# Performance work log

Measured on AMD Instinct MI355X. Metric: run time of the kernel, lower is better.

## Reference

```python
import jax, jax.numpy as jnp
import numpy as np
from jax import lax

NC = 32
EPS = 1e-12


def unfold3x3(x):
    # x: [B,C,H,W] -> [B, C*9, H*W], matching F.unfold(kernel=3, padding=1)
    B, C, H, W = x.shape
    xp = jnp.pad(x, ((0, 0), (0, 0), (1, 1), (1, 1)))
    patches = jnp.stack([xp[:, :, i:i + H, j:j + W]
                         for i in range(3) for j in range(3)], axis=2)  # [B,C,9,H,W]
    return patches.reshape(B, C * 9, H * W)


def fold3x3(u, H, W):
    # u: [B, C*9, H*W] -> [B, C, H, W], matching F.fold(kernel=3, padding=1)
    B = u.shape[0]
    C = u.shape[1] // 9
    p = u.reshape(B, C, 3, 3, H, W)
    out = jnp.zeros((B, C, H + 2, W + 2), u.dtype)
    for i in range(3):
        for j in range(3):
            out = out.at[:, :, i:i + H, j:j + W].add(p[:, :, i, j])
    return out[:, :, 1:H + 1, 1:W + 1]


def l2norm(x, axis):
    n = jnp.sqrt(jnp.sum(x * x, axis=axis, keepdims=True))
    return x / jnp.maximum(n, EPS)


def conv3x3(x, w, b):
    y = lax.conv_general_dilated(x, w, (1, 1), 'SAME',
                                 dimension_numbers=('NCHW', 'OIHW', 'NCHW'))
    return y + b[None, :, None, None]


def setup_inputs() -> dict:
    key = jax.random.key(0)
    k = jax.random.split(key, 6)
    B, C, H, W = 2, NC, 80, 80
    in_HSI = jax.random.normal(k[0], (B, C, H, W), jnp.float32)
    in_PAN = jax.random.normal(k[1], (B, C, H, W), jnp.float32)
    fan1 = 2 * C * 9
    fan2 = C * 9
    w1 = jax.random.normal(k[2], (C, 2 * C, 3, 3), jnp.float32) / np.sqrt(fan1)
    b1 = jax.random.normal(k[3], (C,), jnp.float32) * 0.01
    w2 = jax.random.normal(k[4], (C, C, 3, 3), jnp.float32) / np.sqrt(fan2)
    b2 = jax.random.normal(k[5], (C,), jnp.float32) * 0.01
    return {"in_HSI": in_HSI, "in_PAN": in_PAN, "w1": w1, "b1": b1, "w2": w2, "b2": b2}


def reference(in_HSI, in_PAN, w1, b1, w2, b2):
    B, C, H, W = in_HSI.shape
    L = H * W
    HSI_unfold = unfold3x3(in_HSI)                      # [B, C*9, L]
    PAN_unfold = unfold3x3(in_PAN)                      # [B, C*9, L]
    PAN_q = l2norm(jnp.transpose(PAN_unfold, (0, 2, 1)), axis=2)  # [B, L, C*9]
    HSI_k = l2norm(HSI_unfold, axis=1)                  # [B, C*9, L]
    R = jnp.einsum('blc,bcm->blm', PAN_q, HSI_k)        # [B, L, L]
    R_star = jnp.max(R, axis=1)                         # [B, L]
    R_arg = jnp.argmax(R, axis=1)                       # [B, L]
    # gather columns of unfold(in_PAN) selected by 1-NN indices
    T_unfold = jnp.take_along_axis(PAN_unfold, R_arg[:, None, :], axis=2)
    T_lv3 = fold3x3(T_unfold, H, W) / 9.0               # [B, C, H, W]
    S = R_star.reshape(B, 1, H, W)
    h = jax.nn.relu(conv3x3(jnp.concatenate([T_lv3, in_HSI], axis=1), w1, b1))
    res = conv3x3(h, w2, b2) * S + in_HSI
    return res
```

## Files before the change

### kernel.cpp

```cpp
#include <hip/hip_runtime.h>
#include <hip/hip_bf16.h>
#include <hip/hip_fp16.h>
#include <stdint.h>

#define HH 80
#define WW 80
#define LL 6400
#define CC 32
#define BB 2
#define COG 16
#define DELTA 0.011f
#define NT8 800

typedef __bf16 bf16x8 __attribute__((ext_vector_type(8)));
typedef float  f32x4  __attribute__((ext_vector_type(4)));

__device__ __forceinline__ int div80(int v) {
    return (int)(((unsigned)v * 52429u) >> 22);
}

__device__ __forceinline__ unsigned short f2bf(float f) {
    unsigned int u = __float_as_uint(f);
    return (unsigned short)((u + 0x7fffu + ((u >> 16) & 1u)) >> 16);
}

__device__ __forceinline__ void gload_lds16(void* g, void* l) {
    __builtin_amdgcn_global_load_lds(
        (__attribute__((address_space(1))) void*)g,
        (__attribute__((address_space(3))) void*)l, 16, 0, 0);
}

__global__ void prep1_kernel(const float* __restrict__ HSI, const float* __restrict__ PAN,
                             float* __restrict__ partH, float* __restrict__ partP) {
    int g = blockIdx.x * 256 + threadIdx.x;
    if (g >= BB * CC * LL) return;
    int l = g % LL;
    int y = div80(l), x = l - y * 80;
    const float* hc = HSI + (size_t)(g - l);
    const float* pc = PAN + (size_t)(g - l);
    float sh = 0.f, sp = 0.f;
    #pragma unroll
    for (int i = 0; i < 3; ++i) {
        int yy = y + i - 1;
        if ((unsigned)yy >= 80u) continue;
        #pragma unroll
        for (int j = 0; j < 3; ++j) {
            int xx = x + j - 1;
            if ((unsigned)xx >= 80u) continue;
            float hv = hc[yy * 80 + xx]; sh = fmaf(hv, hv, sh);
            float pv = pc[yy * 80 + xx]; sp = fmaf(pv, pv, sp);
        }
    }
    partH[g] = sh;
    partP[g] = sp;
}

__global__ void prep2_kernel(const float* __restrict__ partH, const float* __restrict__ partP,
                             float* __restrict__ invH, float* __restrict__ invP) {
    int g = blockIdx.x * 256 + threadIdx.x;
    if (g >= BB * LL) return;
    int b = g / LL, l = g - b * LL;
    float sh = 0.f, sp = 0.f;
    #pragma unroll
    for (int c = 0; c < CC; ++c) {
        sh += partH[((size_t)(b * CC + c)) * LL + l];
        sp += partP[((size_t)(b * CC + c)) * LL + l];
    }
    invH[g] = 1.f / fmaxf(sqrtf(sh), 1e-12f);
    invP[g] = 1.f / fmaxf(sqrtf(sp), 1e-12f);
}

__global__ void pack_kernel(const float* __restrict__ HSI, const float* __restrict__ PAN,
                            const float* __restrict__ invH, const float* __restrict__ invP,
                            char* __restrict__ Apack, char* __restrict__ Bpack,
                            float* __restrict__ PANunf, float* __restrict__ HSIunf) {
    int t = blockIdx.x * 256 + threadIdx.x;
    if (t >= BB * 2 * LL * 36) return;
    int g = t % 36;
    int rest = t / 36;
    int l = rest % LL; rest /= LL;
    int mat = rest & 1;
    int b = rest >> 1;
    const float* img = (mat ? HSI : PAN) + (size_t)b * CC * LL;
    float inv = (mat ? invH : invP)[b * LL + l];
    int y = div80(l), x = l - y * 80;
    int k0 = g * 8;
    int c = k0 / 9, tap = k0 - c * 9;
    unsigned short hs[8];
    float raw[8];
    #pragma unroll
    for (int j = 0; j < 8; ++j) {
        int t3 = tap / 3;
        int dy = t3 - 1, dx = tap - t3 * 3 - 1;
        int yy = y + dy, xx = x + dx;
        float rv = ((unsigned)yy < 80u && (unsigned)xx < 80u)
                       ? img[(size_t)c * LL + yy * 80 + xx] : 0.f;
        raw[j] = rv;
        hs[j] = f2bf(rv * inv);
        if (++tap == 9) { tap = 0; ++c; }
    }
    float* unf = (mat ? HSIunf : PANunf) + ((size_t)b * LL + l) * 288 + k0;
    float4 r0 = {raw[0], raw[1], raw[2], raw[3]};
    float4 r1 = {raw[4], raw[5], raw[6], raw[7]};
    *(float4*)(unf)     = r0;
    *(float4*)(unf + 4) = r1;
    char* pk = mat ? Bpack : Apack;
    int slot = (g % 12) ^ (l & 15);
    int q = g / 12;
    size_t off = ((size_t)(b * 3 + q) * LL + l) * 256 + slot * 16;
    uint4 hv;
    hv.x = hs[0] | ((unsigned)hs[1] << 16); hv.y = hs[2] | ((unsigned)hs[3] << 16);
    hv.z = hs[4] | ((unsigned)hs[5] << 16); hv.w = hs[6] | ((unsigned)hs[7] << 16);
    *(uint4*)(pk + off) = hv;
}

__global__ __launch_bounds__(256, 2) void simq_kernel(const char* __restrict__ Apack,
                                                      const char* __restrict__ Bpack,
                                                      __half* __restrict__ tileMax8) {
    __shared__ __align__(16) char Alds[2][32768];
    const int orig = blockIdx.x;
    const int xcd = orig & 7, idx = orig >> 3;
    const int wg = (xcd < 4 ? xcd * 63 : 252 + (xcd - 4) * 62) + idx;
    const int b = wg / 250;
    int rest = wg - b * 250;
    const int sp = rest / 50;
    const int mt = rest - sp * 50;

    const int tid = threadIdx.x;
    const int lane = tid & 63, w = tid >> 6;
    const int wl = w >> 1, wm = w & 1;
    const int r15 = lane & 15, h = lane >> 4;
    const char* Ab = Apack + (size_t)b * 3 * LL * 256;
    const char* Bb = Bpack + (size_t)b * 3 * LL * 256;
    const int m0 = mt * 128;
    const f32x4 fzero = {0.f, 0.f, 0.f, 0.f};

    bf16x8 bq[3][3][4];
    {
        const int rowb = m0 + wm * 64 + r15;
        #pragma unroll
        for (int c = 0; c < 3; ++c)
            #pragma unroll
            for (int ks = 0; ks < 3; ++ks)
                #pragma unroll
                for (int fm = 0; fm < 4; ++fm) {
                    const int gp = ((ks * 4 + h) ^ r15) * 16;
                    bq[c][ks][fm] = *(const bf16x8*)(Bb + ((size_t)c * LL + rowb + fm * 16) * 256 + gp);
                }
    }

    {
        const char* gA = Ab + ((size_t)(sp * 10) * 128) * 256 + w * 8192 + lane * 16;
        char* lA = Alds[0] + w * 8192;
        #pragma unroll
        for (int i = 0; i < 8; ++i) gload_lds16((void*)(gA + i * 1024), lA + i * 1024);
    }
    __syncthreads();

    int cur = 0;
    #pragma unroll 1
    for (int lt = 0; lt < 10; ++lt) {
        f32x4 acc[4][4];
        #pragma unroll
        for (int i = 0; i < 4; ++i)
            #pragma unroll
            for (int j = 0; j < 4; ++j) acc[i][j] = fzero;

        #pragma unroll
        for (int c = 0; c < 3; ++c) {
            if (c < 2 || lt < 9) {
                const int lt2 = (c == 2) ? lt + 1 : lt;
                const int c2  = (c == 2) ? 0 : c + 1;
                const int l0n = (sp * 10 + lt2) * 128;
                const char* gA = Ab + ((size_t)c2 * LL + l0n) * 256 + w * 8192 + lane * 16;
                char* lA = Alds[cur ^ 1] + w * 8192;
                #pragma unroll
                for (int i = 0; i < 8; ++i) gload_lds16((void*)(gA + i * 1024), lA + i * 1024);
            }
            const char* lAr = Alds[cur];
            #pragma unroll
            for (int ks = 0; ks < 3; ++ks) {
                const int gp = ((ks * 4 + h) ^ r15) * 16;
                bf16x8 af[4];
                #pragma unroll
                for (int f = 0; f < 4; ++f)
                    af[f] = *(const bf16x8*)(lAr + (wl * 64 + f * 16 + r15) * 256 + gp);
                #pragma unroll
                for (int fl = 0; fl < 4; ++fl)
                    #pragma unroll
                    for (int fm = 0; fm < 4; ++fm)
                        acc[fl][fm] = __builtin_amdgcn_mfma_f32_16x16x32_bf16(
                            af[fl], bq[c][ks][fm], acc[fl][fm], 0, 0, 0);
            }
            __syncthreads();
            cur ^= 1;
        }

        const int Tbase = (sp * 10 + lt) * 16 + wl * 8;
        #pragma unroll
        for (int fl = 0; fl < 4; ++fl) {
            #pragma unroll
            for (int fm = 0; fm < 4; ++fm) {
                f32x4 a = acc[fl][fm];
                float v = fmaxf(fmaxf(a[0], a[1]), fmaxf(a[2], a[3]));
                v = fmaxf(v, __shfl_xor(v, 16, 64));
                if ((h & 1) == 0) {
                    const int m = m0 + wm * 64 + fm * 16 + r15;
                    tileMax8[((size_t)b * LL + m) * NT8 + Tbase + fl * 2 + (h >> 1)] = __float2half(v);
                }
            }
        }
    }
}

__global__ __launch_bounds__(256) void scanfix_kernel(const float* __restrict__ PANunf,
                                                      const float* __restrict__ HSIunf,
                                                      const float* __restrict__ invH,
                                                      const float* __restrict__ invP,
                                                      const __half* __restrict__ tileMax8,
                                                      float* __restrict__ Sv, int* __restrict__ Sa) {
    const int gw = blockIdx.x * 4 + (threadIdx.x >> 6);
    const int lane = threadIdx.x & 63;
    const int b = gw / LL;
    const __half* tm = tileMax8 + (size_t)gw * NT8;

    float tv[13];
    #pragma unroll
    for (int i = 0; i < 13; ++i) {
        int T = i * 64 + lane;
        tv[i] = (T < NT8) ? __half2float(tm[T]) : -3.0e38f;
    }
    float v1 = tv[0];
    #pragma unroll
    for (int i = 1; i < 13; ++i) v1 = fmaxf(v1, tv[i]);
    #pragma unroll
    for (int d = 1; d < 64; d <<= 1) v1 = fmaxf(v1, __shfl_xor(v1, d, 64));
    const float th = v1 - DELTA;

    const float ihm = invH[gw];
    const int lql = lane >> 3, kq = lane & 7;

    float hreg[36];
    {
        const float4* hv4 = (const float4*)(HSIunf + (size_t)gw * 288 + kq * 36);
        #pragma unroll
        for (int j = 0; j < 9; ++j) {
            float4 v = hv4[j];
            hreg[j * 4 + 0] = v.x; hreg[j * 4 + 1] = v.y;
            hreg[j * 4 + 2] = v.z; hreg[j * 4 + 3] = v.w;
        }
    }

    float bv = -3.0e38f; int bl = 0x7fffffff;

    #pragma unroll 1
    for (int i = 0; i < 13; ++i) {
        unsigned long long mask = __ballot(tv[i] >= th);
        while (mask) {
            const int t = __ffsll((long long)mask) - 1;
            mask &= mask - 1;
            const int T = i * 64 + t;
            const int l = T * 8 + lql;
            const float4* pv4 = (const float4*)(PANunf + ((size_t)b * LL + l) * 288 + kq * 36);
            float part = 0.f;
            #pragma unroll
            for (int j = 0; j < 9; ++j) {
                float4 p = pv4[j];
                part = fmaf(p.x, hreg[j * 4 + 0], part);
                part = fmaf(p.y, hreg[j * 4 + 1], part);
                part = fmaf(p.z, hreg[j * 4 + 2], part);
                part = fmaf(p.w, hreg[j * 4 + 3], part);
            }
            part += __shfl_xor(part, 1, 64);
            part += __shfl_xor(part, 2, 64);
            part += __shfl_xor(part, 4, 64);
            const float val = part * invP[b * LL + l] * ihm;
            if (val > bv || (val == bv && l < bl)) { bv = val; bl = l; }
        }
    }
    #pragma unroll
    for (int d = 1; d < 64; d <<= 1) {
        float ov = __shfl_xor(bv, d, 64);
        int   ol = __shfl_xor(bl, d, 64);
        if (ov > bv || (ov == bv && ol < bl)) { bv = ov; bl = ol; }
    }
    if (lane == 0) { Sv[gw] = bv; Sa[gw] = bl; }
}

__global__ void tfold_kernel(const float* __restrict__ PAN, const int* __restrict__ Sa,
                             float* __restrict__ T) {
    int g = blockIdx.x * blockDim.x + threadIdx.x;
    if (g >= BB * CC * LL) return;
    int bc = g / LL, l = g - bc * LL;
    int b = bc >> 5;
    int y = div80(l), x = l - y * 80;
    const float* img = PAN + (size_t)bc * LL;
    const int* Sab = Sa + b * LL;
    float acc = 0.f;
    #pragma unroll
    for (int i = 0; i < 3; ++i) {
        int yp = y + 1 - i;
        if ((unsigned)yp >= 80u) continue;
        #pragma unroll
        for (int j = 0; j < 3; ++j) {
            int xp = x + 1 - j;
            if ((unsigned)xp >= 80u) continue;
            int a = Sab[yp * 80 + xp];
            int ya = div80(a), xa = a - ya * 80;
            int py = ya + i - 1, px = xa + j - 1;
            if ((unsigned)py < 80u && (unsigned)px < 80u) acc += img[py * 80 + px];
        }
    }
    T[g] = acc * (1.f / 9.f);
}

__global__ __launch_bounds__(256) void conv1_kernel(const float* __restrict__ T,
                                                    const float* __restrict__ HSI,
                                                    const float* __restrict__ w1,
                                                    const float* __restrict__ b1,
                                                    float* __restrict__ h) {
    __shared__ __align__(16) float wl[64][9][COG];
    const int tid = threadIdx.x;
    const int co0 = blockIdx.y * COG;
    for (int idx = tid; idx < 64 * 9 * COG; idx += 256) {
        int cog = idx & (COG - 1);
        int rest = idx >> 4;
        int cin = rest / 9, tap = rest - cin * 9;
        wl[cin][tap][cog] = w1[(co0 + cog) * (64 * 9) + cin * 9 + tap];
    }
    __syncthreads();
    const int g = blockIdx.x * 256 + tid;
    const int b = g / LL, l = g - b * LL;
    const int y = div80(l), x = l - y * 80;
    float acc[COG];
    #pragma unroll
    for (int i = 0; i < COG; ++i) acc[i] = 0.f;
    for (int cin = 0; cin < 64; ++cin) {
        const float* img = (cin < CC) ? (T + (size_t)(b * CC + cin) * LL)
                                      : (HSI + (size_t)(b * CC + (cin - CC)) * LL);
        float tap[9];
        #pragma unroll
        for (int i = 0; i < 3; ++i)
            #pragma unroll
            for (int j = 0; j < 3; ++j) {
                int yy = y + i - 1, xx = x + j - 1;
                tap[i * 3 + j] = ((unsigned)yy < 80u && (unsigned)xx < 80u) ? img[yy * 80 + xx] : 0.f;
            }
        #pragma unroll
        for (int t9 = 0; t9 < 9; ++t9) {
            #pragma unroll
            for (int q4 = 0; q4 < COG / 4; ++q4) {
                const float4 wv = *reinterpret_cast<const float4*>(&wl[cin][t9][q4 * 4]);
                acc[q4 * 4 + 0] = fmaf(tap[t9], wv.x, acc[q4 * 4 + 0]);
                acc[q4 * 4 + 1] = fmaf(tap[t9], wv.y, acc[q4 * 4 + 1]);
                acc[q4 * 4 + 2] = fmaf(tap[t9], wv.z, acc[q4 * 4 + 2]);
                acc[q4 * 4 + 3] = fmaf(tap[t9], wv.w, acc[q4 * 4 + 3]);
            }
        }
    }
    #pragma unroll
    for (int cog = 0; cog < COG; ++cog) {
        float v = acc[cog] + b1[co0 + cog];
        h[(size_t)(b * CC + co0 + cog) * LL + l] = fmaxf(v, 0.f);
    }
}

__global__ __launch_bounds__(256) void conv2_kernel(const float* __restrict__ hbuf,
                                                    const float* __restrict__ HSI,
                                                    const float* __restrict__ Sv,
                                                    const float* __restrict__ w2,
                                                    const float* __restrict__ b2,
                                                    float* __restrict__ out) {
    __shared__ __align__(16) float wl[CC][9][COG];
    const int tid = threadIdx.x;
    const int co0 = blockIdx.y * COG;
    for (int idx = tid; idx < CC * 9 * COG; idx += 256) {
        int cog = idx & (COG - 1);
        int rest = idx >> 4;
        int cin = rest / 9, tap = rest - cin * 9;
        wl[cin][tap][cog] = w2[(co0 + cog) * (CC * 9) + cin * 9 + tap];
    }
    __syncthreads();
    const int g = blockIdx.x * 256 + tid;
    const int b = g / LL, l = g - b * LL;
    const int y = div80(l), x = l - y * 80;
    float acc[COG];
    #pragma unroll
    for (int i = 0; i < COG; ++i) acc[i] = 0.f;
    for (int cin = 0; cin < CC; ++cin) {
        const float* img = hbuf + (size_t)(b * CC + cin) * LL;
        float tap[9];
        #pragma unroll
        for (int i = 0; i < 3; ++i)
            #pragma unroll
            for (int j = 0; j < 3; ++j) {
                int yy = y + i - 1, xx = x + j - 1;
                tap[i * 3 + j] = ((unsigned)yy < 80u && (unsigned)xx < 80u) ? img[yy * 80 + xx] : 0.f;
            }
        #pragma unroll
        for (int t9 = 0; t9 < 9; ++t9) {
            #pragma unroll
            for (int q4 = 0; q4 < COG / 4; ++q4) {
                const float4 wv = *reinterpret_cast<const float4*>(&wl[cin][t9][q4 * 4]);
                acc[q4 * 4 + 0] = fmaf(tap[t9], wv.x, acc[q4 * 4 + 0]);
                acc[q4 * 4 + 1] = fmaf(tap[t9], wv.y, acc[q4 * 4 + 1]);
                acc[q4 * 4 + 2] = fmaf(tap[t9], wv.z, acc[q4 * 4 + 2]);
                acc[q4 * 4 + 3] = fmaf(tap[t9], wv.w, acc[q4 * 4 + 3]);
            }
        }
    }
    const float s = Sv[b * LL + l];
    #pragma unroll
    for (int cog = 0; cog < COG; ++cog) {
        int c = co0 + cog;
        out[(size_t)(b * CC + c) * LL + l] = fmaf(acc[cog] + b2[c], s, HSI[(size_t)(b * CC + c) * LL + l]);
    }
}

extern "C" void kernel_launch(void* const* d_in, const int* in_sizes, int n_in,
                              void* d_out, int out_size, void* d_ws, size_t ws_size,
                              hipStream_t stream) {
    const float* HSI = (const float*)d_in[0];
    const float* PAN = (const float*)d_in[1];
    const float* w1  = (const float*)d_in[2];
    const float* b1  = (const float*)d_in[3];
    const float* w2  = (const float*)d_in[4];
    const float* b2  = (const float*)d_in[5];
    float* out = (float*)d_out;

    char* ws = (char*)d_ws;
    size_t off = 0;
    auto alloc = [&](size_t bytes) -> void* {
        void* p = ws + off;
        off += (bytes + 255) & ~(size_t)255;
        return p;
    };
    float* partH = (float*)alloc((size_t)BB * CC * LL * 4);
    float* partP = (float*)alloc((size_t)BB * CC * LL * 4);
    float* invH  = (float*)alloc((size_t)BB * LL * 4);
    float* invP  = (float*)alloc((size_t)BB * LL * 4);
    char*  Apack = (char*) alloc((size_t)BB * 3 * LL * 256);
    char*  Bpack = (char*) alloc((size_t)BB * 3 * LL * 256);
    __half* tileMax8 = (__half*)alloc((size_t)BB * LL * NT8 * 2);
    float* PANunf = (float*)alloc((size_t)BB * LL * 288 * 4);
    float* HSIunf = (float*)alloc((size_t)BB * LL * 288 * 4);
    float* Sv    = (float*)alloc((size_t)BB * LL * 4);
    int*   Sa    = (int*)  alloc((size_t)BB * LL * 4);
    float* T     = partH;
    float* hbuf  = partP;

    prep1_kernel<<<dim3((BB * CC * LL + 255) / 256), 256, 0, stream>>>(HSI, PAN, partH, partP);
    prep2_kernel<<<dim3((BB * LL + 255) / 256), 256, 0, stream>>>(partH, partP, invH, invP);
    pack_kernel<<<dim3((BB * 2 * LL * 36 + 255) / 256), 256, 0, stream>>>(HSI, PAN, invH, invP,
                                                                          Apack, Bpack, PANunf, HSIunf);
    simq_kernel<<<dim3(500), 256, 0, stream>>>(Apack, Bpack, tileMax8);
    scanfix_kernel<<<dim3(BB * LL / 4), 256, 0, stream>>>(PANunf, HSIunf, invH, invP, tileMax8, Sv, Sa);
    tfold_kernel<<<dim3((BB * CC * LL + 255) / 256), 256, 0, stream>>>(PAN, Sa, T);
    conv1_kernel<<<dim3(BB * LL / 256, CC / COG), 256, 0, stream>>>(T, HSI, w1, b1, hbuf);
    conv2_kernel<<<dim3(BB * LL / 256, CC / COG), 256, 0, stream>>>(hbuf, HSI, Sv, w2, b2, out);
}
```

Before: 226.8 us.

## Split pack into unfold and bf16 pack kernels; replace simq syncthreads with fine-grained waitcnt barriers

```diff
diff --git a/kernel.cpp b/kernel.cpp
--- a/kernel.cpp
+++ b/kernel.cpp
@@ -70,40 +70,49 @@
     invP[g] = 1.f / fmaxf(sqrtf(sp), 1e-12f);
 }
 
-__global__ void pack_kernel(const float* __restrict__ HSI, const float* __restrict__ PAN,
-                            const float* __restrict__ invH, const float* __restrict__ invP,
-                            char* __restrict__ Apack, char* __restrict__ Bpack,
-                            float* __restrict__ PANunf, float* __restrict__ HSIunf) {
+__global__ void unfold_kernel(const float* __restrict__ HSI, const float* __restrict__ PAN,
+                              float* __restrict__ PANunf, float* __restrict__ HSIunf) {
+    int t = blockIdx.x * 256 + threadIdx.x;
+    if (t >= BB * 2 * CC * LL) return;
+    int l = t % LL;
+    int rc = t / LL;
+    int c = rc & (CC - 1);
+    int bm = rc >> 5;
+    int mat = bm & 1, b = bm >> 1;
+    const float* img = (mat ? HSI : PAN) + ((size_t)b * CC + c) * LL;
+    float* unf = (mat ? HSIunf : PANunf) + ((size_t)b * LL + l) * 288 + c * 9;
+    int y = div80(l), x = l - y * 80;
+    #pragma unroll
+    for (int dy = 0; dy < 3; ++dy) {
+        int yy = y + dy - 1;
+        #pragma unroll
+        for (int dx = 0; dx < 3; ++dx) {
+            int xx = x + dx - 1;
+            float v = ((unsigned)yy < 80u && (unsigned)xx < 80u) ? img[yy * 80 + xx] : 0.f;
+            unf[dy * 3 + dx] = v;
+        }
+    }
+}
+
+__global__ void packbf16_kernel(const float* __restrict__ PANunf, const float* __restrict__ HSIunf,
+                                const float* __restrict__ invH, const float* __restrict__ invP,
+                                char* __restrict__ Apack, char* __restrict__ Bpack) {
     int t = blockIdx.x * 256 + threadIdx.x;
     if (t >= BB * 2 * LL * 36) return;
     int g = t % 36;
     int rest = t / 36;
-    int l = rest % LL; rest /= LL;
-    int mat = rest & 1;
-    int b = rest >> 1;
-    const float* img = (mat ? HSI : PAN) + (size_t)b * CC * LL;
+    int l = rest % LL;
+    int bm = rest / LL;
+    int mat = bm & 1, b = bm >> 1;
+    const float* unf = (mat ? HSIunf : PANunf) + ((size_t)b * LL + l) * 288 + g * 8;
     float inv = (mat ? invH : invP)[b * LL + l];
-    int y = div80(l), x = l - y * 80;
-    int k0 = g * 8;
-    int c = k0 / 9, tap = k0 - c * 9;
+    float4 r0 = *(const float4*)(unf);
+    float4 r1 = *(const float4*)(unf + 4);
     unsigned short hs[8];
-    float raw[8];
-    #pragma unroll
-    for (int j = 0; j < 8; ++j) {
-        int t3 = tap / 3;
-        int dy = t3 - 1, dx = tap - t3 * 3 - 1;
-        int yy = y + dy, xx = x + dx;
-        float rv = ((unsigned)yy < 80u && (unsigned)xx < 80u)
-                       ? img[(size_t)c * LL + yy * 80 + xx] : 0.f;
-        raw[j] = rv;
-        hs[j] = f2bf(rv * inv);
-        if (++tap == 9) { tap = 0; ++c; }
-    }
-    float* unf = (mat ? HSIunf : PANunf) + ((size_t)b * LL + l) * 288 + k0;
-    float4 r0 = {raw[0], raw[1], raw[2], raw[3]};
-    float4 r1 = {raw[4], raw[5], raw[6], raw[7]};
-    *(float4*)(unf)     = r0;
-    *(float4*)(unf + 4) = r1;
+    hs[0] = f2bf(r0.x * inv); hs[1] = f2bf(r0.y * inv);
+    hs[2] = f2bf(r0.z * inv); hs[3] = f2bf(r0.w * inv);
+    hs[4] = f2bf(r1.x * inv); hs[5] = f2bf(r1.y * inv);
+    hs[6] = f2bf(r1.z * inv); hs[7] = f2bf(r1.w * inv);
     char* pk = mat ? Bpack : Apack;
     int slot = (g % 12) ^ (l & 15);
     int q = g / 12;
@@ -149,17 +158,20 @@
                 }
     }
 
+    const char* gAbase = Ab + w * 8192 + lane * 16;
+    char* lA0 = Alds[0] + w * 8192;
+    char* lA1 = Alds[1] + w * 8192;
+
     {
-        const char* gA = Ab + ((size_t)(sp * 10) * 128) * 256 + w * 8192 + lane * 16;
-        char* lA = Alds[0] + w * 8192;
-        #pragma unroll
-        for (int i = 0; i < 8; ++i) gload_lds16((void*)(gA + i * 1024), lA + i * 1024);
-    }
-    __syncthreads();
+        const char* gA = gAbase + ((size_t)(sp * 10) * 128) * 256;
+        #pragma unroll
+        for (int i = 0; i < 8; ++i) gload_lds16((void*)(gA + i * 1024), lA0 + i * 1024);
+    }
 
     int cur = 0;
     #pragma unroll 1
     for (int lt = 0; lt < 10; ++lt) {
+        const int l0 = (sp * 10 + lt) * 128;
         f32x4 acc[4][4];
         #pragma unroll
         for (int i = 0; i < 4; ++i)
@@ -169,14 +181,19 @@
         #pragma unroll
         for (int c = 0; c < 3; ++c) {
             if (c < 2 || lt < 9) {
-                const int lt2 = (c == 2) ? lt + 1 : lt;
-                const int c2  = (c == 2) ? 0 : c + 1;
-                const int l0n = (sp * 10 + lt2) * 128;
-                const char* gA = Ab + ((size_t)c2 * LL + l0n) * 256 + w * 8192 + lane * 16;
-                char* lA = Alds[cur ^ 1] + w * 8192;
+                const int c2  = (c + 1) % 3;
+                const int l0n = (c == 2) ? l0 + 128 : l0;
+                const char* gA = gAbase + ((size_t)c2 * LL + l0n) * 256;
+                char* lA = cur ? lA1 : lA0;
+                lA = (cur ^ 1) ? lA1 : lA0;
                 #pragma unroll
                 for (int i = 0; i < 8; ++i) gload_lds16((void*)(gA + i * 1024), lA + i * 1024);
-            }
+                asm volatile("s_waitcnt vmcnt(8)" ::: "memory");
+            } else {
+                asm volatile("s_waitcnt vmcnt(0)" ::: "memory");
+            }
+            __builtin_amdgcn_s_barrier();
+            asm volatile("" ::: "memory");
             const char* lAr = Alds[cur];
             #pragma unroll
             for (int ks = 0; ks < 3; ++ks) {
@@ -192,7 +209,9 @@
                         acc[fl][fm] = __builtin_amdgcn_mfma_f32_16x16x32_bf16(
                             af[fl], bq[c][ks][fm], acc[fl][fm], 0, 0, 0);
             }
-            __syncthreads();
+            asm volatile("s_waitcnt lgkmcnt(0)" ::: "memory");
+            __builtin_amdgcn_s_barrier();
+            asm volatile("" ::: "memory");
             cur ^= 1;
         }
 
@@ -451,8 +470,9 @@
 
     prep1_kernel<<<dim3((BB * CC * LL + 255) / 256), 256, 0, stream>>>(HSI, PAN, partH, partP);
     prep2_kernel<<<dim3((BB * LL + 255) / 256), 256, 0, stream>>>(partH, partP, invH, invP);
-    pack_kernel<<<dim3((BB * 2 * LL * 36 + 255) / 256), 256, 0, stream>>>(HSI, PAN, invH, invP,
-                                                                          Apack, Bpack, PANunf, HSIunf);
+    unfold_kernel<<<dim3((BB * 2 * CC * LL + 255) / 256), 256, 0, stream>>>(HSI, PAN, PANunf, HSIunf);
+    packbf16_kernel<<<dim3((BB * 2 * LL * 36 + 255) / 256), 256, 0, stream>>>(PANunf, HSIunf, invH, invP,
+                                                                              Apack, Bpack);
     simq_kernel<<<dim3(500), 256, 0, stream>>>(Apack, Bpack, tileMax8);
     scanfix_kernel<<<dim3(BB * LL / 4), 256, 0, stream>>>(PANunf, HSIunf, invH, invP, tileMax8, Sv, Sa);
     tfold_kernel<<<dim3((BB * CC * LL + 255) / 256), 256, 0, stream>>>(PAN, Sa, T);
```

Measured after the change: 314.3 us. 1.39x slower.
